# Kernel tuning notes

Measured on AMD Instinct MI355X. Metric: run time of the kernel, lower is better.

The kernel has to match this reference:

```python
import jax, jax.numpy as jnp
import numpy as np

D_MODEL = 2048
N_HEADS = 16
N_KV = 4
HEAD_DIM = 128
SUB = 64
WINDOW = 512
THETA = 10000.0
NEG = jnp.float32(-1e30)


def _rope_tables(seq_len):
    inv_freq = 1.0 / (THETA ** (jnp.arange(0, HEAD_DIM, 2, dtype=jnp.float32) / HEAD_DIM))
    freqs = jnp.arange(seq_len, dtype=jnp.float32)[:, None] * inv_freq[None, :]  # [S, hd/2]
    emb = jnp.concatenate([freqs, freqs], axis=-1)  # [S, hd]
    return jnp.cos(emb), jnp.sin(emb)


def _rotate_half(x):
    x1, x2 = x[..., : HEAD_DIM // 2], x[..., HEAD_DIM // 2 :]
    return jnp.concatenate([-x2, x1], axis=-1)


def _apply_rope(t, cos, sin):
    # t: [B, H, S, hd]; cos/sin: [S, hd]
    c = cos[None, None]
    s = sin[None, None]
    return t * c + _rotate_half(t) * s


def setup_inputs() -> dict:
    key = jax.random.key(0)
    ks = jax.random.split(key, 6)
    B, S = 1, 2048
    std = 0.02
    return {
        "x": jax.random.normal(ks[0], (B, S, D_MODEL), dtype=jnp.float32),
        "Wq": jax.random.normal(ks[1], (D_MODEL, N_HEADS * HEAD_DIM), dtype=jnp.float32) * std,
        "Wk": jax.random.normal(ks[2], (D_MODEL, N_KV * HEAD_DIM), dtype=jnp.float32) * std,
        "Wv": jax.random.normal(ks[3], (D_MODEL, N_KV * HEAD_DIM), dtype=jnp.float32) * std,
        "Wo": jax.random.normal(ks[4], (N_HEADS * HEAD_DIM, D_MODEL), dtype=jnp.float32) * std,
        "lam": jnp.full((N_HEADS,), 0.1, dtype=jnp.float32),
    }


def reference(x, Wq, Wk, Wv, Wo, lam):
    B, S, _ = x.shape
    n_rep = N_HEADS // N_KV

    q = (x @ Wq).reshape(B, S, N_HEADS, HEAD_DIM).transpose(0, 2, 1, 3)  # [B,H,S,hd]
    k = (x @ Wk).reshape(B, S, N_KV, HEAD_DIM).transpose(0, 2, 1, 3)    # [B,KH,S,hd]
    v = (x @ Wv).reshape(B, S, N_KV, HEAD_DIM).transpose(0, 2, 1, 3)

    cos, sin = _rope_tables(S)
    q = _apply_rope(q, cos, sin)
    k = _apply_rope(k, cos, sin)

    # GQA repeat: each kv head replicated n_rep times consecutively
    k = jnp.repeat(k, n_rep, axis=1)  # [B,H,S,hd]
    v = jnp.repeat(v, n_rep, axis=1)

    q1, q2 = q[..., :SUB], q[..., SUB:]
    k1, k2 = k[..., :SUB], k[..., SUB:]
    scale = 1.0 / jnp.sqrt(jnp.float32(SUB))

    s1 = jnp.einsum("bhqd,bhkd->bhqk", q1, k1) * scale
    s2 = jnp.einsum("bhqd,bhkd->bhqk", q2, k2) * scale

    i = jnp.arange(S)[:, None]
    j = jnp.arange(S)[None, :]
    allowed = (j <= i) & (j >= i - WINDOW + 1)  # causal + sliding window
    s1 = jnp.where(allowed[None, None], s1, NEG)
    s2 = jnp.where(allowed[None, None], s2, NEG)

    a1 = jax.nn.softmax(s1.astype(jnp.float32), axis=-1).astype(x.dtype)
    a2 = jax.nn.softmax(s2.astype(jnp.float32), axis=-1).astype(x.dtype)

    diff = jax.nn.relu(a1 - lam[None, :, None, None] * a2)
    diff = diff / (jnp.sum(diff, axis=-1, keepdims=True) + 1e-6)

    out = jnp.einsum("bhqk,bhkd->bhqd", diff, v)  # [B,H,S,hd]
    out = out.transpose(0, 2, 1, 3).reshape(B, S, N_HEADS * HEAD_DIM)
    return out @ Wo
```

## Files before the change

### kernel.cpp

```cpp
#include <hip/hip_runtime.h>
#include <hip/hip_bf16.h>
#include <stdint.h>

typedef __attribute__((ext_vector_type(8))) short short8;
typedef __attribute__((ext_vector_type(4))) float f32x4;
using bf16 = __hip_bfloat16;

#define MFMA16(a, b, c) __builtin_amdgcn_mfma_f32_16x16x32_bf16((a), (b), (c), 0, 0, 0)

#define GLOAD_LDS16(g, l) __builtin_amdgcn_global_load_lds( \
    (const __attribute__((address_space(1))) void*)(g),     \
    (__attribute__((address_space(3))) void*)(l), 16, 0, 0)

__device__ __forceinline__ unsigned packbf2(float lo, float hi) {
  unsigned r;
  asm("v_cvt_pk_bf16_f32 %0, %1, %2" : "=v"(r) : "v"(lo), "v"(hi));
  return r;
}
__device__ __forceinline__ float ex2(float x) {
  float r;
  asm("v_exp_f32 %0, %1" : "=v"(r) : "v"(x));
  return r;
}

template <bool EDGE>
__device__ __forceinline__ void p1s(const f32x4* sv, float& l,
                                    int kb0, int myq, int lhi) {
  float sum = 0.f;
#pragma unroll
  for (int nt = 0; nt < 4; ++nt) {
    float part = 0.f;
#pragma unroll
    for (int r = 0; r < 4; ++r) {
      float e = ex2(sv[nt][r]);
      if (EDGE) {
        int key = kb0 + nt * 16 + lhi * 4 + r;
        bool ok = (key <= myq) && (key > myq - 512);
        e = ok ? e : 0.f;
      }
      part += e;
    }
    sum += part;
  }
  l += sum;
}

template <bool EDGE>
__device__ __forceinline__ float p2s(const f32x4* s1v, const f32x4* s2v,
                                     float c2, int kb0, int myq, int lhi, int l15,
                                     unsigned* pw) {
  float d0 = 0.f, d1 = 0.f;
#pragma unroll
  for (int nt = 0; nt < 4; ++nt) {
    float pr[4];
#pragma unroll
    for (int r = 0; r < 4; ++r) {
      float e1 = ex2(s1v[nt][r]);
      float e2 = ex2(s2v[nt][r]);
      float p = fmaf(-c2, e2, e1);
      p = fmaxf(p, 0.f);
      if (EDGE) {
        int key = kb0 + nt * 16 + lhi * 4 + r;
        bool ok = (key <= myq) && (key > myq - 512);
        p = ok ? p : 0.f;
      }
      pr[r] = p;
      if (r & 1) d1 += p; else d0 += p;
    }
    int pi = l15 * 36 + 8 * nt + 2 * lhi;
    pw[pi]     = packbf2(pr[0], pr[1]);
    pw[pi + 1] = packbf2(pr[2], pr[3]);
  }
  return d0 + d1;
}

__global__ __launch_bounds__(256) void prep_all(const float* __restrict__ x,
                                                const float* __restrict__ Wq,
                                                const float* __restrict__ Wk,
                                                const float* __restrict__ Wv,
                                                const float* __restrict__ Wo,
                                                bf16* __restrict__ xb,
                                                bf16* __restrict__ WqkvFT,
                                                bf16* __restrict__ WoFT)
{
  const int bx = blockIdx.x;
  const int tid = threadIdx.x;
  if (bx >= 80) {
    size_t i = ((size_t)(bx - 80) * 32 + blockIdx.y) * 2048 + tid * 8;
    const float* f = x + i;
    float4 a = *(const float4*)f;
    float4 b = *(const float4*)(f + 4);
    union { bf16 h[8]; short8 s; } u;
    u.h[0] = __float2bfloat16(a.x); u.h[1] = __float2bfloat16(a.y);
    u.h[2] = __float2bfloat16(a.z); u.h[3] = __float2bfloat16(a.w);
    u.h[4] = __float2bfloat16(b.x); u.h[5] = __float2bfloat16(b.y);
    u.h[6] = __float2bfloat16(b.z); u.h[7] = __float2bfloat16(b.w);
    *(short8*)(xb + i) = u.s;
    return;
  }
  const float* W;
  bf16* Wt;
  int N, n0;
  if (bx < 32)      { W = Wq; Wt = WqkvFT; N = 2048; n0 = bx * 64; }
  else if (bx < 40) { W = Wk; Wt = WqkvFT; N = 512;  n0 = 2048 + (bx - 32) * 64; }
  else if (bx < 48) { W = Wv; Wt = WqkvFT; N = 512;  n0 = 2560 + (bx - 40) * 64; }
  else              { W = Wo; Wt = WoFT;   N = 2048; n0 = (bx - 48) * 64; }
  const int nloc0 = (N == 512) ? (n0 - ((n0 >= 2560) ? 2560 : 2048)) : ((bx < 32 || bx >= 48) ? (n0 & 2047) : 0);
  const int k0 = blockIdx.y * 64;

  __shared__ bf16 t[64][72];
#pragma unroll
  for (int pass = 0; pass < 4; ++pass) {
    int r = pass * 16 + (tid >> 4);
    int c = (tid & 15) * 4;
    float4 v = *(const float4*)(W + (size_t)(k0 + r) * N + nloc0 + c);
    t[c + 0][r] = __float2bfloat16(v.x);
    t[c + 1][r] = __float2bfloat16(v.y);
    t[c + 2][r] = __float2bfloat16(v.z);
    t[c + 3][r] = __float2bfloat16(v.w);
  }
  __syncthreads();
#pragma unroll
  for (int pass = 0; pass < 2; ++pass) {
    int n = pass * 32 + (tid >> 3);
    int k8 = (tid & 7) * 8;
    int frag = ((n0 + n) >> 4) * 64 + ((k0 + k8) >> 5);
    int ln = (n & 15) + 16 * ((k8 >> 3) & 3);
    *(short8*)(Wt + (size_t)frag * 512 + ln * 8) = *(const short8*)(&t[n][k8]);
  }
}

__global__ __launch_bounds__(512) void gemm_qkv(const bf16* __restrict__ A,
                                                const bf16* __restrict__ Bft,
                                                bf16* __restrict__ QKV,
                                                bf16* __restrict__ VTp,
                                                int M, int N, int K)
{
  __shared__ __align__(16) char smem[65536];
  bf16* As = (bf16*)smem;

  const int tid  = threadIdx.x;
  const int lane = tid & 63;
  const int w    = tid >> 6;
  const int wmg  = (w >> 2) * 4;
  const int wng  = (w & 3) * 4;
  const int l15  = lane & 15;
  const int lhi  = lane >> 4;

  const int nbx = gridDim.x;
  const int lb  = blockIdx.y * nbx + blockIdx.x;
  const int nwg = nbx * gridDim.y;
  const int lsw = (lb & 7) * (nwg >> 3) + (lb >> 3);
  const int bm0 = (lsw / nbx) * 128;
  const int bn0 = (lsw % nbx) * 256;

  const int srow = tid >> 2;
  const int scol = ((tid & 3) ^ ((tid >> 3) & 3)) * 8;
  const int loff = l15 * 4 + (lhi ^ ((l15 >> 1) & 3));

  const int nkc = K >> 5;
  const bf16* bbase[4];
#pragma unroll
  for (int nt = 0; nt < 4; ++nt)
    bbase[nt] = Bft + ((size_t)((bn0 >> 4) + wng + nt) * nkc) * 512 + lane * 8;

  f32x4 acc[4][4];
  const f32x4 zero4 = {0.f, 0.f, 0.f, 0.f};
#pragma unroll
  for (int i = 0; i < 4; ++i)
#pragma unroll
    for (int j = 0; j < 4; ++j) acc[i][j] = zero4;

  short8 br0[4], br1[4], br2[4], br3[4];

#define GSTAGE_A(buf, kk)                                                           \
  { GLOAD_LDS16(A + (size_t)(bm0 + srow) * K + (kk) + scol,                         \
                As + (buf) * 4096 + tid * 8); }

#define BLOAD(breg, kc)                                                             \
  { _Pragma("unroll")                                                               \
    for (int nt = 0; nt < 4; ++nt) {                                                \
      asm volatile("global_load_dwordx4 %0, %1, off"                                \
                   : "=v"(breg[nt])                                                 \
                   : "v"(bbase[nt] + (size_t)(kc) * 512)                            \
                   : "memory");                                                     \
    } }

#define KSTEP(aslot, breg, wcn, ...)                                                \
  {                                                                                 \
    asm volatile("s_waitcnt vmcnt(" #wcn ")" ::: "memory");                         \
    __builtin_amdgcn_s_barrier();                                                   \
    __builtin_amdgcn_sched_barrier(0);                                              \
    __VA_ARGS__                                                                     \
    short8 a_[4];                                                                   \
    _Pragma("unroll")                                                               \
    for (int mt = 0; mt < 4; ++mt)                                                  \
      a_[mt] = *(const short8*)(As + (aslot) * 4096 + ((wmg + mt) * 64 + loff) * 8);\
    _Pragma("unroll")                                                               \
    for (int mt = 0; mt < 4; ++mt)                                                  \
      _Pragma("unroll")                                                             \
      for (int nt = 0; nt < 4; ++nt)                                                \
        acc[mt][nt] = MFMA16(a_[mt], breg[nt], acc[mt][nt]);                        \
  }

  GSTAGE_A(0, 0);  BLOAD(br0, 0);
  GSTAGE_A(1, 32); BLOAD(br1, 1);
  GSTAGE_A(2, 64); BLOAD(br2, 2);

  for (int t = 0; t < nkc - 4; t += 4) {
    KSTEP(0, br0, 10, GSTAGE_A(3, (t + 3) * 32); BLOAD(br3, t + 3);)
    KSTEP(1, br1, 10, GSTAGE_A(0, (t + 4) * 32); BLOAD(br0, t + 4);)
    KSTEP(2, br2, 10, GSTAGE_A(1, (t + 5) * 32); BLOAD(br1, t + 5);)
    KSTEP(3, br3, 10, GSTAGE_A(2, (t + 6) * 32); BLOAD(br2, t + 6);)
  }
  KSTEP(0, br0, 10, GSTAGE_A(3, (nkc - 1) * 32); BLOAD(br3, nkc - 1);)
  KSTEP(1, br1, 10, )
  KSTEP(2, br2, 5, )
  KSTEP(3, br3, 0, )
#undef GSTAGE_A
#undef BLOAD
#undef KSTEP

  __syncthreads();
  if (bn0 < 2560) {
    float* Lf = (float*)smem;
    const float scale = (bn0 < 2048) ? 0.180336880111120f : 1.0f;
#pragma unroll
    for (int half = 0; half < 2; ++half) {
      if ((w >> 2) == half) {
#pragma unroll
        for (int mt = 0; mt < 4; ++mt)
#pragma unroll
          for (int nt = 0; nt < 4; ++nt) {
            int col = (w & 3) * 64 + nt * 16 + l15;
#pragma unroll
            for (int r = 0; r < 4; ++r)
              Lf[(mt * 16 + lhi * 4 + r) * 256 + col] = acc[mt][nt][r];
          }
      }
      __syncthreads();
      {
        int row = tid >> 3;
        int pg = (tid & 7) * 16;
        int head = pg >> 6;
        int din0 = pg & 63;
        int col1 = head * 128 + din0;
        int s = bm0 + half * 64 + row;
        bf16* orow = QKV + (size_t)s * 3072 + bn0;
        union { bf16 h[16]; short8 v[2]; } o1, o2;
#pragma unroll
        for (int e = 0; e < 16; ++e) {
          int din = din0 + e;
          float inv = __expf(-(float)din * (9.210340371976184f / 64.0f));
          float ang = (float)s * inv;
          float cs = __cosf(ang), sn = __sinf(ang);
          float x1 = Lf[row * 256 + col1 + e];
          float x2 = Lf[row * 256 + col1 + e + 64];
          o1.h[e] = __float2bfloat16((x1 * cs - x2 * sn) * scale);
          o2.h[e] = __float2bfloat16((x2 * cs + x1 * sn) * scale);
        }
        *(short8*)(orow + col1)      = o1.v[0];
        *(short8*)(orow + col1 + 8)  = o1.v[1];
        *(short8*)(orow + col1 + 64) = o2.v[0];
        *(short8*)(orow + col1 + 72) = o2.v[1];
      }
      __syncthreads();
    }
  } else {
    const int dimbase = (bn0 - 2560) + (w & 3) * 64;
#pragma unroll
    for (int mt = 0; mt < 4; ++mt) {
#pragma unroll
      for (int nt = 0; nt < 4; ++nt) {
        int dim = dimbase + nt * 16 + l15;
        int key0 = bm0 + (w >> 2) * 64 + mt * 16 + lhi * 4;
        uint2 pk;
        pk.x = packbf2(acc[mt][nt][0], acc[mt][nt][1]);
        pk.y = packbf2(acc[mt][nt][2], acc[mt][nt][3]);
        *(uint2*)(VTp + (size_t)dim * 2048 + key0) = pk;
      }
    }
  }
}

__global__ __launch_bounds__(256) void gemm_wo(const bf16* __restrict__ A,
                                               const bf16* __restrict__ Bft,
                                               float* __restrict__ C,
                                               int M, int N, int K)
{
  __shared__ __align__(16) bf16 As[4][128 * 32];

  const int tid  = threadIdx.x;
  const int lane = tid & 63;
  const int w    = tid >> 6;
  const int wmg  = (w >> 1) * 4;
  const int wng  = (w & 1) * 4;
  const int l15  = lane & 15;
  const int lhi  = lane >> 4;

  const int nbx = gridDim.x;
  const int lb  = blockIdx.y * nbx + blockIdx.x;
  const int nwg = nbx * gridDim.y;
  const int lsw = (lb & 7) * (nwg >> 3) + (lb >> 3);
  const int bm0 = (lsw / nbx) * 128;
  const int bn0 = (lsw % nbx) * 128;

  const int srow = lane >> 2;
  const int scol = ((lane & 3) ^ ((lane >> 3) & 3)) * 8;
  const int loff = l15 * 4 + (lhi ^ ((l15 >> 1) & 3));

  const int nkc = K >> 5;
  const bf16* bbase[4];
#pragma unroll
  for (int nt = 0; nt < 4; ++nt)
    bbase[nt] = Bft + ((size_t)((bn0 >> 4) + wng + nt) * nkc) * 512 + lane * 8;

  f32x4 acc[4][4];
  const f32x4 zero4 = {0.f, 0.f, 0.f, 0.f};
#pragma unroll
  for (int i = 0; i < 4; ++i)
#pragma unroll
    for (int j = 0; j < 4; ++j) acc[i][j] = zero4;

  short8 br0[4], br1[4], br2[4], br3[4];

#define GSTAGE_A(buf, kk)                                                          \
  { _Pragma("unroll")                                                              \
    for (int p = 0; p < 2; ++p) {                                                  \
      int s   = (p * 4 + w) * 64 + lane;                                           \
      int row = (p * 4 + w) * 16 + srow;                                           \
      GLOAD_LDS16(A + (size_t)(bm0 + row) * K + (kk) + scol, &As[buf][s * 8]);     \
    } }

#define BLOAD(breg, kc)                                                            \
  { _Pragma("unroll")                                                              \
    for (int nt = 0; nt < 4; ++nt) {                                               \
      asm volatile("global_load_dwordx4 %0, %1, off"                               \
                   : "=v"(breg[nt])                                                \
                   : "v"(bbase[nt] + (size_t)(kc) * 512)                           \
                   : "memory");                                                    \
    } }

#define KSTEP(aslot, breg, wcn, ...)                                               \
  {                                                                                \
    asm volatile("s_waitcnt vmcnt(" #wcn ")" ::: "memory");                        \
    __builtin_amdgcn_s_barrier();                                                  \
    __builtin_amdgcn_sched_barrier(0);                                             \
    __VA_ARGS__                                                                    \
    short8 a_[4];                                                                  \
    _Pragma("unroll")                                                              \
    for (int mt = 0; mt < 4; ++mt)                                                 \
      a_[mt] = *(const short8*)(&As[aslot][((wmg + mt) * 64 + loff) * 8]);         \
    _Pragma("unroll")                                                              \
    for (int mt = 0; mt < 4; ++mt)                                                 \
      _Pragma("unroll")                                                            \
      for (int nt = 0; nt < 4; ++nt)                                               \
        acc[mt][nt] = MFMA16(a_[mt], breg[nt], acc[mt][nt]);                       \
  }

  GSTAGE_A(0, 0);  BLOAD(br0, 0);
  GSTAGE_A(1, 32); BLOAD(br1, 1);
  GSTAGE_A(2, 64); BLOAD(br2, 2);

  for (int t = 0; t < nkc - 4; t += 4) {
    KSTEP(0, br0, 12, GSTAGE_A(3, (t + 3) * 32); BLOAD(br3, t + 3);)
    KSTEP(1, br1, 12, GSTAGE_A(0, (t + 4) * 32); BLOAD(br0, t + 4);)
    KSTEP(2, br2, 12, GSTAGE_A(1, (t + 5) * 32); BLOAD(br1, t + 5);)
    KSTEP(3, br3, 12, GSTAGE_A(2, (t + 6) * 32); BLOAD(br2, t + 6);)
  }
  KSTEP(0, br0, 12, GSTAGE_A(3, (nkc - 1) * 32); BLOAD(br3, nkc - 1);)
  KSTEP(1, br1, 12, )
  KSTEP(2, br2, 6, )
  KSTEP(3, br3, 0, )
#undef GSTAGE_A
#undef BLOAD
#undef KSTEP

#pragma unroll
  for (int mt = 0; mt < 4; ++mt) {
    int row0 = bm0 + (wmg + mt) * 16 + lhi * 4;
#pragma unroll
    for (int nt = 0; nt < 4; ++nt) {
      int col = bn0 + (wng + nt) * 16 + l15;
#pragma unroll
      for (int r = 0; r < 4; ++r)
        C[(size_t)(row0 + r) * N + col] = acc[mt][nt][r];
    }
  }
}

__global__ __launch_bounds__(256) void diff_attn(const bf16* __restrict__ QKV,
                                                 const bf16* __restrict__ VT,
                                                 const float* __restrict__ lam,
                                                 bf16* __restrict__ O)
{
  __shared__ __align__(16) bf16 Kb[2][64 * 128];
  __shared__ __align__(16) bf16 Vb[2][128 * 64];
  __shared__ __align__(16) bf16 Pw[4][16 * 72];

  const int lb  = blockIdx.y * 32 + blockIdx.x;
  const int lsw = (lb & 7) * 64 + (lb >> 3);
  const int qb  = lsw & 31;
  const int h   = lsw >> 5;

  const int kvh  = h >> 2;
  const int tid  = threadIdx.x;
  const int lane = tid & 63;
  const int w    = tid >> 6;
  const int l15  = lane & 15;
  const int lhi  = lane >> 4;
  const int qg   = qb * 64 + w * 16;
  const int myq  = qg + l15;
  const float lamv = lam[h];

  const bf16* Kg = QKV + 2048 + (size_t)kvh * 128;
  const bf16* Vg = VT + (size_t)kvh * 128 * 2048;

  short8 qf[4];
  {
    const bf16* qrow = QKV + (size_t)myq * 3072 + h * 128;
#pragma unroll
    for (int c = 0; c < 4; ++c)
      qf[c] = *(const short8*)(qrow + c * 32 + lhi * 8);
  }

  const int t0 = (qb >= 8) ? (qb - 8) : 0;

#define STAGE_K(buf, kbase)                                                     \
  {                                                                             \
    _Pragma("unroll")                                                           \
    for (int p = 0; p < 4; ++p) {                                               \
      int c = p * 256 + tid;                                                    \
      int r = c >> 4, q = c & 15;                                               \
      GLOAD_LDS16(Kg + (size_t)((kbase) + r) * 3072 + ((q ^ (r & 7)) * 8),      \
                  &Kb[buf][c * 8]);                                             \
    }                                                                           \
  }
#define STAGE_V(buf, kbase)                                                     \
  {                                                                             \
    _Pragma("unroll")                                                           \
    for (int p = 0; p < 4; ++p) {                                               \
      int c = p * 256 + tid;                                                    \
      int d = c >> 3, q = c & 7;                                                \
      GLOAD_LDS16(Vg + (size_t)d * 2048 + (kbase) + ((q ^ (d & 7)) * 8),        \
                  &Vb[buf][c * 8]);                                             \
    }                                                                           \
  }
#define KFRAG(buf, nt, qc) \
  (*(const short8*)(&Kb[buf][(((nt) * 16 + l15) * 16 + ((qc) ^ (((nt) * 16 + l15) & 7))) * 8]))
#define VFRAG(buf, n, qc) \
  (*(const short8*)(&Vb[buf][(((n) * 16 + l15) * 8 + ((qc) ^ (((n) * 16 + l15) & 7))) * 8]))
#define QK_TILE(cur)                                            \
  _Pragma("unroll")                                             \
  for (int nt = 0; nt < 4; ++nt) {                              \
    f32x4 s1 = zero4, s2 = zero4;                               \
    s1 = MFMA16(KFRAG(cur, nt, lhi),      qf[0], s1);           \
    s1 = MFMA16(KFRAG(cur, nt, 4 + lhi),  qf[1], s1);           \
    s2 = MFMA16(KFRAG(cur, nt, 8 + lhi),  qf[2], s2);           \
    s2 = MFMA16(KFRAG(cur, nt, 12 + lhi), qf[3], s2);           \
    s1v[nt] = s1; s2v[nt] = s2;                                 \
  }

  const f32x4 zero4 = {0.f, 0.f, 0.f, 0.f};

  float l1 = 0.f, l2 = 0.f;
  STAGE_K(0, t0 * 64);
  asm volatile("s_waitcnt vmcnt(0)" ::: "memory");
  __builtin_amdgcn_s_barrier();
  {
    int cur = 0;
    for (int t = t0; t <= qb; ++t, cur ^= 1) {
      if (t < qb) {
        STAGE_K(cur ^ 1, (t + 1) * 64);
        asm volatile("s_waitcnt vmcnt(4)" ::: "memory");
      } else {
        asm volatile("s_waitcnt vmcnt(0)" ::: "memory");
      }
      __builtin_amdgcn_s_barrier();
      __builtin_amdgcn_sched_barrier(0);
      const int kb0 = t * 64;
      f32x4 s1v[4], s2v[4];
      QK_TILE(cur);
      const bool edge = (t == qb) || (qb >= 8 && t == t0);
      if (edge) {
        p1s<true>(s1v, l1, kb0, myq, lhi);
        p1s<true>(s2v, l2, kb0, myq, lhi);
      } else {
        p1s<false>(s1v, l1, kb0, myq, lhi);
        p1s<false>(s2v, l2, kb0, myq, lhi);
      }
      __builtin_amdgcn_s_barrier();
    }
  }

  l1 += __shfl_xor(l1, 16, 64);
  l1 += __shfl_xor(l1, 32, 64);
  l2 += __shfl_xor(l2, 16, 64);
  l2 += __shfl_xor(l2, 32, 64);
  const float c2 = lamv * l1 / l2;

  f32x4 accv[8];
#pragma unroll
  for (int n = 0; n < 8; ++n) accv[n] = zero4;
  float dln = 0.f;

  STAGE_K(0, t0 * 64);
  STAGE_V(0, t0 * 64);
  asm volatile("s_waitcnt vmcnt(0)" ::: "memory");
  __builtin_amdgcn_s_barrier();
  {
    int cur = 0;
    for (int t = t0; t <= qb; ++t, cur ^= 1) {
      if (t < qb) {
        STAGE_K(cur ^ 1, (t + 1) * 64);
        STAGE_V(cur ^ 1, (t + 1) * 64);
        asm volatile("s_waitcnt vmcnt(8)" ::: "memory");
      } else {
        asm volatile("s_waitcnt vmcnt(0)" ::: "memory");
      }
      __builtin_amdgcn_s_barrier();
      __builtin_amdgcn_sched_barrier(0);
      const int kb0 = t * 64;
      unsigned* pw = (unsigned*)&Pw[w][0];
      f32x4 s1v[4], s2v[4];
      QK_TILE(cur);
      const bool edge = (t == qb) || (qb >= 8 && t == t0);
      if (edge) dln += p2s<true>(s1v, s2v, c2, kb0, myq, lhi, l15, pw);
      else      dln += p2s<false>(s1v, s2v, c2, kb0, myq, lhi, l15, pw);
#pragma unroll
      for (int kc = 0; kc < 2; ++kc) {
        short8 pa = *(const short8*)(&Pw[w][l15 * 72 + kc * 32 + lhi * 8]);
#pragma unroll
        for (int n = 0; n < 8; ++n)
          accv[n] = MFMA16(pa, VFRAG(cur, n, kc * 4 + lhi), accv[n]);
      }
      __builtin_amdgcn_s_barrier();
    }
  }

  dln += __shfl_xor(dln, 16, 64);
  dln += __shfl_xor(dln, 32, 64);

#pragma unroll
  for (int r = 0; r < 4; ++r) {
    int srcq = lhi * 4 + r;
    int src = (lane & 48) | srcq;
    float dq = __shfl(dln, src, 64);
    float lq = __shfl(l1, src, 64);
    float rinv = 1.f / (dq + lq * 1e-6f);
    int qo = qg + srcq;
#pragma unroll
    for (int n = 0; n < 8; ++n) {
      O[(size_t)qo * 2048 + h * 128 + n * 16 + l15] =
          __float2bfloat16(accv[n][r] * rinv);
    }
  }
#undef STAGE_K
#undef STAGE_V
#undef KFRAG
#undef VFRAG
#undef QK_TILE
}

extern "C" void kernel_launch(void* const* d_in, const int* in_sizes, int n_in,
                              void* d_out, int out_size, void* d_ws, size_t ws_size,
                              hipStream_t stream)
{
  const float* x   = (const float*)d_in[0];
  const float* Wq  = (const float*)d_in[1];
  const float* Wk  = (const float*)d_in[2];
  const float* Wv  = (const float*)d_in[3];
  const float* Wo  = (const float*)d_in[4];
  const float* lam = (const float*)d_in[5];

  char* ws = (char*)d_ws;
  bf16* xb     = (bf16*)(ws);
  bf16* WqkvFT = (bf16*)(ws + 8ull  * (1u << 20));
  bf16* WoFT   = (bf16*)(ws + 20ull * (1u << 20));
  bf16* QKV    = (bf16*)(ws + 28ull * (1u << 20));
  bf16* ATT    = (bf16*)(ws + 40ull * (1u << 20));
  bf16* VT     = (bf16*)(ws + 48ull * (1u << 20));

  prep_all<<<dim3(144, 32), 256, 0, stream>>>(x, Wq, Wk, Wv, Wo, xb, WqkvFT, WoFT);
  gemm_qkv<<<dim3(12, 16), 512, 0, stream>>>(xb, WqkvFT, QKV, VT, 2048, 3072, 2048);
  diff_attn<<<dim3(32, 16), 256, 0, stream>>>(QKV, VT, lam, ATT);
  gemm_wo<<<dim3(16, 16), 256, 0, stream>>>(ATT, WoFT, (float*)d_out, 2048, 2048, 2048);
}
```

Baseline: 104.7 us.

## Use 128x192 QKV GEMM tiles with permuted head-dim layout for rope

Shrinks the QKV GEMM N-tile from 256 to 192 columns, which raises the grid from 192 to 256 workgroups so it fills the GPU's CUs more evenly. Because 192-wide tiles no longer align with 128-wide heads, the Q/K weight columns are permuted at prep time so that each 64-column chunk holds paired rotate-half partners 32 apart. The rope epilogue works in this permuted layout, and the attention kernel's MFMA fragment pairing is swapped to match. The cost is more complex epilogue indexing and per-element branching, plus fewer MFMAs per B load.

New measurement: 103.9 us. About the same (-0.8%).

```diff
diff --git a/kernel.cpp b/kernel.cpp
--- a/kernel.cpp
+++ b/kernel.cpp
@@ -100,11 +100,11 @@
   }
   const float* W;
   bf16* Wt;
-  int N, n0;
-  if (bx < 32)      { W = Wq; Wt = WqkvFT; N = 2048; n0 = bx * 64; }
-  else if (bx < 40) { W = Wk; Wt = WqkvFT; N = 512;  n0 = 2048 + (bx - 32) * 64; }
-  else if (bx < 48) { W = Wv; Wt = WqkvFT; N = 512;  n0 = 2560 + (bx - 40) * 64; }
-  else              { W = Wo; Wt = WoFT;   N = 2048; n0 = (bx - 48) * 64; }
+  int N, n0, prm;
+  if (bx < 32)      { W = Wq; Wt = WqkvFT; N = 2048; n0 = bx * 64;               prm = 1; }
+  else if (bx < 40) { W = Wk; Wt = WqkvFT; N = 512;  n0 = 2048 + (bx - 32) * 64; prm = 1; }
+  else if (bx < 48) { W = Wv; Wt = WqkvFT; N = 512;  n0 = 2560 + (bx - 40) * 64; prm = 0; }
+  else              { W = Wo; Wt = WoFT;   N = 2048; n0 = (bx - 48) * 64;        prm = 0; }
   const int nloc0 = (N == 512) ? (n0 - ((n0 >= 2560) ? 2560 : 2048)) : ((bx < 32 || bx >= 48) ? (n0 & 2047) : 0);
   const int k0 = blockIdx.y * 64;
 
@@ -124,8 +124,14 @@
   for (int pass = 0; pass < 2; ++pass) {
     int n = pass * 32 + (tid >> 3);
     int k8 = (tid & 7) * 8;
-    int frag = ((n0 + n) >> 4) * 64 + ((k0 + k8) >> 5);
-    int ln = (n & 15) + 16 * ((k8 >> 3) & 3);
+    int ng = n0 + n;
+    if (prm) {
+      int d = ng & 127;
+      int dp = (d & 31) | ((d & 32) << 1) | ((d & 64) >> 1);
+      ng = (ng & ~127) | dp;
+    }
+    int frag = (ng >> 4) * 64 + ((k0 + k8) >> 5);
+    int ln = (ng & 15) + 16 * ((k8 >> 3) & 3);
     *(short8*)(Wt + (size_t)frag * 512 + ln * 8) = *(const short8*)(&t[n][k8]);
   }
 }
@@ -143,7 +149,7 @@
   const int lane = tid & 63;
   const int w    = tid >> 6;
   const int wmg  = (w >> 2) * 4;
-  const int wng  = (w & 3) * 4;
+  const int wn3  = (w & 3) * 3;
   const int l15  = lane & 15;
   const int lhi  = lane >> 4;
 
@@ -152,26 +158,26 @@
   const int nwg = nbx * gridDim.y;
   const int lsw = (lb & 7) * (nwg >> 3) + (lb >> 3);
   const int bm0 = (lsw / nbx) * 128;
-  const int bn0 = (lsw % nbx) * 256;
+  const int bn0 = (lsw % nbx) * 192;
 
   const int srow = tid >> 2;
   const int scol = ((tid & 3) ^ ((tid >> 3) & 3)) * 8;
   const int loff = l15 * 4 + (lhi ^ ((l15 >> 1) & 3));
 
   const int nkc = K >> 5;
-  const bf16* bbase[4];
-#pragma unroll
-  for (int nt = 0; nt < 4; ++nt)
-    bbase[nt] = Bft + ((size_t)((bn0 >> 4) + wng + nt) * nkc) * 512 + lane * 8;
-
-  f32x4 acc[4][4];
+  const bf16* bbase[3];
+#pragma unroll
+  for (int nt = 0; nt < 3; ++nt)
+    bbase[nt] = Bft + ((size_t)((bn0 >> 4) + wn3 + nt) * nkc) * 512 + lane * 8;
+
+  f32x4 acc[4][3];
   const f32x4 zero4 = {0.f, 0.f, 0.f, 0.f};
 #pragma unroll
   for (int i = 0; i < 4; ++i)
 #pragma unroll
-    for (int j = 0; j < 4; ++j) acc[i][j] = zero4;
-
-  short8 br0[4], br1[4], br2[4], br3[4];
+    for (int j = 0; j < 3; ++j) acc[i][j] = zero4;
+
+  short8 br0[3], br1[3], br2[3], br3[3];
 
 #define GSTAGE_A(buf, kk)                                                           \
   { GLOAD_LDS16(A + (size_t)(bm0 + srow) * K + (kk) + scol,                         \
@@ -179,7 +185,7 @@
 
 #define BLOAD(breg, kc)                                                             \
   { _Pragma("unroll")                                                               \
-    for (int nt = 0; nt < 4; ++nt) {                                                \
+    for (int nt = 0; nt < 3; ++nt) {                                                \
       asm volatile("global_load_dwordx4 %0, %1, off"                                \
                    : "=v"(breg[nt])                                                 \
                    : "v"(bbase[nt] + (size_t)(kc) * 512)                            \
@@ -199,7 +205,7 @@
     _Pragma("unroll")                                                               \
     for (int mt = 0; mt < 4; ++mt)                                                  \
       _Pragma("unroll")                                                             \
-      for (int nt = 0; nt < 4; ++nt)                                                \
+      for (int nt = 0; nt < 3; ++nt)                                                \
         acc[mt][nt] = MFMA16(a_[mt], breg[nt], acc[mt][nt]);                        \
   }
 
@@ -208,76 +214,110 @@
   GSTAGE_A(2, 64); BLOAD(br2, 2);
 
   for (int t = 0; t < nkc - 4; t += 4) {
-    KSTEP(0, br0, 10, GSTAGE_A(3, (t + 3) * 32); BLOAD(br3, t + 3);)
-    KSTEP(1, br1, 10, GSTAGE_A(0, (t + 4) * 32); BLOAD(br0, t + 4);)
-    KSTEP(2, br2, 10, GSTAGE_A(1, (t + 5) * 32); BLOAD(br1, t + 5);)
-    KSTEP(3, br3, 10, GSTAGE_A(2, (t + 6) * 32); BLOAD(br2, t + 6);)
-  }
-  KSTEP(0, br0, 10, GSTAGE_A(3, (nkc - 1) * 32); BLOAD(br3, nkc - 1);)
-  KSTEP(1, br1, 10, )
-  KSTEP(2, br2, 5, )
+    KSTEP(0, br0, 8, GSTAGE_A(3, (t + 3) * 32); BLOAD(br3, t + 3);)
+    KSTEP(1, br1, 8, GSTAGE_A(0, (t + 4) * 32); BLOAD(br0, t + 4);)
+    KSTEP(2, br2, 8, GSTAGE_A(1, (t + 5) * 32); BLOAD(br1, t + 5);)
+    KSTEP(3, br3, 8, GSTAGE_A(2, (t + 6) * 32); BLOAD(br2, t + 6);)
+  }
+  KSTEP(0, br0, 8, GSTAGE_A(3, (nkc - 1) * 32); BLOAD(br3, nkc - 1);)
+  KSTEP(1, br1, 8, )
+  KSTEP(2, br2, 4, )
   KSTEP(3, br3, 0, )
 #undef GSTAGE_A
 #undef BLOAD
 #undef KSTEP
 
   __syncthreads();
-  if (bn0 < 2560) {
+
+  const int ropeW = (bn0 + 192 <= 2560) ? 192 : ((bn0 >= 2560) ? 0 : 64);
+
+  if (ropeW > 0) {
     float* Lf = (float*)smem;
-    const float scale = (bn0 < 2048) ? 0.180336880111120f : 1.0f;
 #pragma unroll
     for (int half = 0; half < 2; ++half) {
       if ((w >> 2) == half) {
 #pragma unroll
         for (int mt = 0; mt < 4; ++mt)
 #pragma unroll
-          for (int nt = 0; nt < 4; ++nt) {
-            int col = (w & 3) * 64 + nt * 16 + l15;
-#pragma unroll
-            for (int r = 0; r < 4; ++r)
-              Lf[(mt * 16 + lhi * 4 + r) * 256 + col] = acc[mt][nt][r];
+          for (int nt = 0; nt < 3; ++nt) {
+            int lc = (wn3 + nt) * 16 + l15;
+            if (lc < ropeW) {
+#pragma unroll
+              for (int r = 0; r < 4; ++r)
+                Lf[(mt * 16 + lhi * 4 + r) * ropeW + lc] = acc[mt][nt][r];
+            }
           }
       }
       __syncthreads();
       {
         int row = tid >> 3;
-        int pg = (tid & 7) * 16;
-        int head = pg >> 6;
-        int din0 = pg & 63;
-        int col1 = head * 128 + din0;
         int s = bm0 + half * 64 + row;
-        bf16* orow = QKV + (size_t)s * 3072 + bn0;
-        union { bf16 h[16]; short8 v[2]; } o1, o2;
-#pragma unroll
-        for (int e = 0; e < 16; ++e) {
-          int din = din0 + e;
-          float inv = __expf(-(float)din * (9.210340371976184f / 64.0f));
-          float ang = (float)s * inv;
-          float cs = __cosf(ang), sn = __sinf(ang);
-          float x1 = Lf[row * 256 + col1 + e];
-          float x2 = Lf[row * 256 + col1 + e + 64];
-          o1.h[e] = __float2bfloat16((x1 * cs - x2 * sn) * scale);
-          o2.h[e] = __float2bfloat16((x2 * cs + x1 * sn) * scale);
+        if (ropeW == 192) {
+          int cg = (tid & 7) * 24;
+          bf16* orow = QKV + (size_t)s * 3072 + bn0 + cg;
+          union { bf16 h[24]; short8 v[3]; } o;
+#pragma unroll
+          for (int e = 0; e < 24; ++e) {
+            int c = cg + e;
+            int g = bn0 + c;
+            int p = g & 127;
+            int w32 = p & 63;
+            int b = p >> 6;
+            int d = b * 32 + (w32 & 31);
+            float scale = (g < 2048) ? 0.180336880111120f : 1.0f;
+            float inv = __expf(-(float)d * (9.210340371976184f / 64.0f));
+            float ang = (float)s * inv;
+            float cs = __cosf(ang), sn = __sinf(ang);
+            bool first = (w32 < 32);
+            float xa = Lf[row * 192 + c];
+            float xb = Lf[row * 192 + (first ? c + 32 : c - 32)];
+            float out = fmaf(first ? -xb : xb, sn, xa * cs);
+            o.h[e] = __float2bfloat16(out * scale);
+          }
+          *(short8*)(orow)      = o.v[0];
+          *(short8*)(orow + 8)  = o.v[1];
+          *(short8*)(orow + 16) = o.v[2];
+        } else {
+          int cg = (tid & 7) * 8;
+          bf16* orow = QKV + (size_t)s * 3072 + bn0 + cg;
+          union { bf16 h[8]; short8 v; } o;
+#pragma unroll
+          for (int e = 0; e < 8; ++e) {
+            int c = cg + e;
+            int g = bn0 + c;
+            int p = g & 127;
+            int w32 = p & 63;
+            int b = p >> 6;
+            int d = b * 32 + (w32 & 31);
+            float inv = __expf(-(float)d * (9.210340371976184f / 64.0f));
+            float ang = (float)s * inv;
+            float cs = __cosf(ang), sn = __sinf(ang);
+            bool first = (w32 < 32);
+            float xa = Lf[row * 64 + c];
+            float xb = Lf[row * 64 + (first ? c + 32 : c - 32)];
+            float out = fmaf(first ? -xb : xb, sn, xa * cs);
+            o.h[e] = __float2bfloat16(out);
+          }
+          *(short8*)(orow) = o.v;
         }
-        *(short8*)(orow + col1)      = o1.v[0];
-        *(short8*)(orow + col1 + 8)  = o1.v[1];
-        *(short8*)(orow + col1 + 64) = o2.v[0];
-        *(short8*)(orow + col1 + 72) = o2.v[1];
       }
       __syncthreads();
     }
-  } else {
-    const int dimbase = (bn0 - 2560) + (w & 3) * 64;
-#pragma unroll
-    for (int mt = 0; mt < 4; ++mt) {
-#pragma unroll
-      for (int nt = 0; nt < 4; ++nt) {
-        int dim = dimbase + nt * 16 + l15;
-        int key0 = bm0 + (w >> 2) * 64 + mt * 16 + lhi * 4;
-        uint2 pk;
-        pk.x = packbf2(acc[mt][nt][0], acc[mt][nt][1]);
-        pk.y = packbf2(acc[mt][nt][2], acc[mt][nt][3]);
-        *(uint2*)(VTp + (size_t)dim * 2048 + key0) = pk;
+  }
+  if (bn0 + 192 > 2560) {
+#pragma unroll
+    for (int nt = 0; nt < 3; ++nt) {
+      int gfc = bn0 + (wn3 + nt) * 16;
+      if (gfc >= 2560) {
+        int dim = gfc - 2560 + l15;
+#pragma unroll
+        for (int mt = 0; mt < 4; ++mt) {
+          int key0 = bm0 + (w >> 2) * 64 + mt * 16 + lhi * 4;
+          uint2 pk;
+          pk.x = packbf2(acc[mt][nt][0], acc[mt][nt][1]);
+          pk.y = packbf2(acc[mt][nt][2], acc[mt][nt][3]);
+          *(uint2*)(VTp + (size_t)dim * 2048 + key0) = pk;
+        }
       }
     }
   }
@@ -455,8 +495,8 @@
   for (int nt = 0; nt < 4; ++nt) {                              \
     f32x4 s1 = zero4, s2 = zero4;                               \
     s1 = MFMA16(KFRAG(cur, nt, lhi),      qf[0], s1);           \
-    s1 = MFMA16(KFRAG(cur, nt, 4 + lhi),  qf[1], s1);           \
-    s2 = MFMA16(KFRAG(cur, nt, 8 + lhi),  qf[2], s2);           \
+    s1 = MFMA16(KFRAG(cur, nt, 8 + lhi),  qf[2], s1);           \
+    s2 = MFMA16(KFRAG(cur, nt, 4 + lhi),  qf[1], s2);           \
     s2 = MFMA16(KFRAG(cur, nt, 12 + lhi), qf[3], s2);           \
     s1v[nt] = s1; s2v[nt] = s2;                                 \
   }
@@ -582,7 +622,7 @@
   bf16* VT     = (bf16*)(ws + 48ull * (1u << 20));
 
   prep_all<<<dim3(144, 32), 256, 0, stream>>>(x, Wq, Wk, Wv, Wo, xb, WqkvFT, WoFT);
-  gemm_qkv<<<dim3(12, 16), 512, 0, stream>>>(xb, WqkvFT, QKV, VT, 2048, 3072, 2048);
+  gemm_qkv<<<dim3(16, 16), 512, 0, stream>>>(xb, WqkvFT, QKV, VT, 2048, 3072, 2048);
   diff_attn<<<dim3(32, 16), 256, 0, stream>>>(QKV, VT, lam, ATT);
   gemm_wo<<<dim3(16, 16), 256, 0, stream>>>(ATT, WoFT, (float*)d_out, 2048, 2048, 2048);
 }
```
